# Kernel tuning notes

Hardware: AMD Instinct MI355X
Metric: run time of the kernel (lower is better)

Reference implementation:

```python
import jax, jax.numpy as jnp
import numpy as np

VOCAB = 50257
D_MODEL = 1024
TOKENS = 4096
K = 64


def setup_inputs() -> dict:
    key = jax.random.key(0)
    k1, k2, k3 = jax.random.split(key, 3)
    x = jax.random.normal(k1, (TOKENS, D_MODEL), dtype=jnp.float32)
    b = jax.random.normal(k2, (VOCAB, D_MODEL), dtype=jnp.float32)
    target = jax.random.randint(k3, (TOKENS,), 0, VOCAB, dtype=jnp.int64)
    return {"x": x, "b": b, "target": target, "k": K}


def reference(x, b, target, k):
    # faiss.knn_gpu with default METRIC_L2 returns the k SMALLEST squared-L2
    # distances D between each query row of x [tokens, d] and the database
    # rows of b [vocab, d]. target is unused in the original forward.
    x_sq = jnp.sum(x * x, axis=1, keepdims=True)          # [tokens, 1]
    b_sq = jnp.sum(b * b, axis=1)                          # [vocab]
    dist = x_sq + b_sq[None, :] - 2.0 * (x @ b.T)          # [tokens, vocab]
    # top-k smallest distances == top-k largest of -dist (sorted ascending)
    neg_d, _ = jax.lax.top_k(-dist, k)                     # [tokens, k]
    return -neg_d
```

## Files before the change

### kernel.cpp

```cpp
#include <hip/hip_runtime.h>
#include <hip/hip_bf16.h>
#include <stdint.h>

#define TOKENS 4096
#define DMODEL 1024
#define VOCAB  50257
#define KSEL   64
#define BM 128
#define BN 128
#define BK 64
#define MTILES (TOKENS / BM)
#define NSPLIT_A 16
#define COLS_A   128
#define SAMPLE_END (NSPLIT_A * COLS_A)
#define NSPLIT_B 16
#define COLS_B (VOCAB - SAMPLE_END)
#define COLS_PER ((COLS_B + NSPLIT_B - 1) / NSPLIT_B)
#define SEG 256
#define CAP 56
#define MERGE_THR 17
#define TSZ (BM * BK)
#define INF __builtin_inff()

typedef unsigned short u16;
typedef long i64;
typedef __attribute__((ext_vector_type(4))) float f32x4;

#define GLOAD16(gp, lp) __builtin_amdgcn_global_load_lds( \
    (const __attribute__((address_space(1))) void*)(gp),  \
    (__attribute__((address_space(3))) void*)(lp), 16, 0, 0)
#define GLOAD4(gp, lp) __builtin_amdgcn_global_load_lds(  \
    (const __attribute__((address_space(1))) void*)(gp),  \
    (__attribute__((address_space(3))) void*)(lp), 4, 0, 0)

#define WAITB(N) do { asm volatile("s_waitcnt vmcnt(" #N ")" ::: "memory"); \
                      __builtin_amdgcn_s_barrier(); } while (0)
#define LBAR() do { asm volatile("s_waitcnt lgkmcnt(0)" ::: "memory"); \
                    __builtin_amdgcn_s_barrier(); } while (0)
#define DRAIN_VM() asm volatile("s_waitcnt vmcnt(0)" ::: "memory")

__global__ __launch_bounds__(256) void prep_kernel(
    const float* __restrict__ x, const float* __restrict__ b,
    uint8_t* __restrict__ xh, uint8_t* __restrict__ bh,
    float* __restrict__ xsq, float* __restrict__ bsq) {
  int row = blockIdx.x;
  int tid = threadIdx.x;
  const float* src;
  uint8_t* dst;
  float* nrm;
  int r;
  if (row < TOKENS) {
    r = row; src = x + (size_t)r * DMODEL; dst = xh + (size_t)r * DMODEL; nrm = xsq;
  } else {
    r = row - TOKENS; src = b + (size_t)r * DMODEL; dst = bh + (size_t)r * DMODEL; nrm = bsq;
  }
  float4 v = reinterpret_cast<const float4*>(src)[tid];
  float s = v.x * v.x + v.y * v.y + v.z * v.z + v.w * v.w;
  uint32_t w = __builtin_amdgcn_cvt_pk_fp8_f32(v.x, v.y, 0, false);
  w = __builtin_amdgcn_cvt_pk_fp8_f32(v.z, v.w, w, true);
  reinterpret_cast<uint32_t*>(dst)[tid] = w;
#pragma unroll
  for (int j = 1; j < 64; j <<= 1) s += __shfl_xor(s, j);
  __shared__ float acc4[4];
  if ((tid & 63) == 0) acc4[tid >> 6] = s;
  __syncthreads();
  if (tid == 0) nrm[r] = acc4[0] + acc4[1] + acc4[2] + acc4[3];
}

__device__ __attribute__((noinline)) float merge_row(float lstv, const float* cb, int cnt) {
  const int lane = threadIdx.x & 63;
  float v0 = (lane < cnt) ? cb[lane] : INF;
#pragma unroll
  for (int k = 2; k <= 64; k <<= 1) {
#pragma unroll
    for (int j = k >> 1; j > 0; j >>= 1) {
      float p = __shfl_xor(v0, j);
      bool keepmin = (((lane & j) == 0) == ((lane & k) == 0));
      v0 = keepmin ? fminf(v0, p) : fmaxf(v0, p);
    }
  }
  float rev = __shfl(v0, 63 - lane);
  float m = fminf(lstv, rev);
#pragma unroll
  for (int j = 32; j > 0; j >>= 1) {
    float p = __shfl_xor(m, j);
    m = ((lane & j) == 0) ? fminf(m, p) : fmaxf(m, p);
  }
  return m;
}

__device__ __forceinline__ float merge64(float a, float b, int lane) {
  float rev = __shfl(b, 63 - lane);
  float m = fminf(a, rev);
#pragma unroll
  for (int j = 32; j > 0; j >>= 1) {
    float p = __shfl_xor(m, j);
    m = ((lane & j) == 0) ? fminf(m, p) : fmaxf(m, p);
  }
  return m;
}

#define STAGE_STEP(BB, KS) do {                        \
    GLOAD16(a_src + (KS), &As[(BB) + wave * 1024]);    \
    GLOAD16(b_src + (KS), &Bs[(BB) + wave * 1024]);    \
  } while (0)

#define MFMA8(a0_, a1_, b0_, b1_, b2_, b3_)                                           \
    acc[0][0] = __builtin_amdgcn_mfma_f32_16x16x32_fp8_fp8(a0_, b0_, acc[0][0], 0, 0, 0); \
    acc[0][1] = __builtin_amdgcn_mfma_f32_16x16x32_fp8_fp8(a0_, b1_, acc[0][1], 0, 0, 0); \
    acc[0][2] = __builtin_amdgcn_mfma_f32_16x16x32_fp8_fp8(a0_, b2_, acc[0][2], 0, 0, 0); \
    acc[0][3] = __builtin_amdgcn_mfma_f32_16x16x32_fp8_fp8(a0_, b3_, acc[0][3], 0, 0, 0); \
    acc[1][0] = __builtin_amdgcn_mfma_f32_16x16x32_fp8_fp8(a1_, b0_, acc[1][0], 0, 0, 0); \
    acc[1][1] = __builtin_amdgcn_mfma_f32_16x16x32_fp8_fp8(a1_, b1_, acc[1][1], 0, 0, 0); \
    acc[1][2] = __builtin_amdgcn_mfma_f32_16x16x32_fp8_fp8(a1_, b2_, acc[1][2], 0, 0, 0); \
    acc[1][3] = __builtin_amdgcn_mfma_f32_16x16x32_fp8_fp8(a1_, b3_, acc[1][3], 0, 0, 0);

#define LD8(arr, BB, off) (*reinterpret_cast<const i64*>(&(arr)[(BB) + (off)]))
#define COMPUTE_STEP(BB) do {                                                  \
    i64 a0 = LD8(As, BB, A00), a1 = LD8(As, BB, A10);                          \
    i64 b0 = LD8(Bs, BB, B00), b1 = LD8(Bs, BB, B10);                          \
    i64 b2 = LD8(Bs, BB, B20), b3 = LD8(Bs, BB, B30);                          \
    __builtin_amdgcn_s_setprio(1);                                             \
    MFMA8(a0, a1, b0, b1, b2, b3)                                              \
    __builtin_amdgcn_s_setprio(0);                                             \
    i64 a0b = LD8(As, BB, A01), a1b = LD8(As, BB, A11);                        \
    i64 b0b = LD8(Bs, BB, B01), b1b = LD8(Bs, BB, B11);                        \
    i64 b2b = LD8(Bs, BB, B21), b3b = LD8(Bs, BB, B31);                        \
    __builtin_amdgcn_s_setprio(1);                                             \
    MFMA8(a0b, a1b, b0b, b1b, b2b, b3b)                                        \
    __builtin_amdgcn_s_setprio(0);                                             \
  } while (0)

#define GEOM_COMMON                                                            \
  const int g4 = lane >> 4, fr = lane & 15;                                    \
  const int wm = wave >> 1, wn = wave & 1;                                     \
  const int rj = g4 * 4;                                                       \
  auto po = [&](int row, int c) {                                              \
    return row * 64 + ((((c >> 4) ^ ((row >> 1) & 3)) << 4) | (c & 15));       \
  };                                                                           \
  const int c0 = g4 * 8, c1 = 32 + g4 * 8;                                     \
  const int rA0 = wm * 32 + fr, rA1 = rA0 + 16;                                \
  const int rB0 = wn * 64 + fr, rB1 = rB0 + 16, rB2 = rB0 + 32, rB3 = rB0 + 48;\
  const int A00 = po(rA0, c0), A01 = po(rA0, c1);                              \
  const int A10 = po(rA1, c0), A11 = po(rA1, c1);                              \
  const int B00 = po(rB0, c0), B01 = po(rB0, c1);                              \
  const int B10 = po(rB1, c0), B11 = po(rB1, c1);                              \
  const int B20 = po(rB2, c0), B21 = po(rB2, c1);                              \
  const int B30 = po(rB3, c0), B31 = po(rB3, c1);

#define K_PIPELINE3()                                                           \
    _Pragma("unroll 1")                                                         \
    for (int i = 0; i < 4; ++i) {                                               \
      const int ksb = i * 192;                                                  \
      WAITB(2); STAGE_STEP(2 * TSZ, ksb + 128); COMPUTE_STEP(0);                \
      WAITB(2); STAGE_STEP(0,       ksb + 192); COMPUTE_STEP(TSZ);              \
      WAITB(2); STAGE_STEP(TSZ,     ksb + 256); COMPUTE_STEP(2 * TSZ);          \
    }                                                                           \
    WAITB(2); STAGE_STEP(2 * TSZ, 896); COMPUTE_STEP(0);                        \
    WAITB(2); STAGE_STEP(0,       960); COMPUTE_STEP(TSZ);                      \
    WAITB(2);                           COMPUTE_STEP(2 * TSZ);                  \
    WAITB(0);                           COMPUTE_STEP(0);

#define K_PIPELINE4()                                                           \
    _Pragma("unroll 1")                                                         \
    for (int i = 0; i < 3; ++i) {                                               \
      const int ksb = i * 256;                                                  \
      WAITB(4); STAGE_STEP(3 * TSZ, ksb + 192); COMPUTE_STEP(0);                \
      WAITB(4); STAGE_STEP(0,       ksb + 256); COMPUTE_STEP(TSZ);              \
      WAITB(4); STAGE_STEP(TSZ,     ksb + 320); COMPUTE_STEP(2 * TSZ);          \
      WAITB(4); STAGE_STEP(2 * TSZ, ksb + 384); COMPUTE_STEP(3 * TSZ);          \
    }                                                                           \
    WAITB(4); STAGE_STEP(3 * TSZ, 960); COMPUTE_STEP(0);              \
    WAITB(4);                           COMPUTE_STEP(TSZ);            \
    WAITB(2);                           COMPUTE_STEP(2 * TSZ);        \
    WAITB(0);                           COMPUTE_STEP(3 * TSZ);

__global__ __launch_bounds__(512, 4) void gemm_topk_sample(
    const uint8_t* __restrict__ xh, const uint8_t* __restrict__ bh,
    const float* __restrict__ xsq, const float* __restrict__ bsqg,
    float* __restrict__ parts) {
  __shared__ uint8_t As[3 * TSZ];
  __shared__ uint8_t Bs[3 * TSZ];
  __shared__ float cbuf[BM][CAP];
  __shared__ float tau[BM];
  __shared__ int   ccnt[BM];
  __shared__ float xsq_s[BM];

  const int tid  = threadIdx.x;
  const int lane = tid & 63;
  const int wave = tid >> 6;
  const int xcd = blockIdx.x & 7, idx = blockIdx.x >> 3;
  const int mt  = xcd * 4 + (idx & 3);
  const int ns  = idx >> 2;

  const int mrow0 = mt * BM;
  const int col0  = ns * COLS_A;
  const int col1  = col0 + COLS_A;

  const int stg_row = wave * 16 + (lane >> 2);
  const int stg_gran = ((lane & 3) ^ ((lane >> 3) & 3)) << 4;
  const uint8_t* a_src = xh + (size_t)(mrow0 + stg_row) * DMODEL + stg_gran;
  const uint8_t* b_src = bh + (size_t)(col0 + stg_row) * DMODEL + stg_gran;

  if (tid < BM) {
    xsq_s[tid] = xsq[mrow0 + tid];
    tau[tid] = INF;
    ccnt[tid] = 0;
  }
  STAGE_STEP(0, 0);
  STAGE_STEP(TSZ, BK);

  float lst[16];
#pragma unroll
  for (int i = 0; i < 16; ++i) lst[i] = INF;

  GEOM_COMMON
  const int r0 = wm * 32 + wn * 16;

  const int cbase = col0;
  f32x4 acc[2][4];
#pragma unroll
  for (int i = 0; i < 2; ++i)
#pragma unroll
    for (int j = 0; j < 4; ++j) acc[i][j] = (f32x4){0.f, 0.f, 0.f, 0.f};

  K_PIPELINE3()

#pragma unroll
  for (int p = 0; p < 4; ++p) {
    if (wn == (p & 1)) {
#pragma unroll
      for (int f2 = 0; f2 < 2; ++f2) {
        const int fn = (p >> 1) * 2 + f2;
        const int c = cbase + wn * 64 + fn * 16 + fr;
        const float bq = bsqg[c];
#pragma unroll
        for (int fm = 0; fm < 2; ++fm) {
#pragma unroll
          for (int j = 0; j < 4; ++j) {
            const int rl = wm * 32 + fm * 16 + rj + j;
            const float dist = xsq_s[rl] + bq - 2.0f * acc[fm][fn][j];
            if (dist < tau[rl]) {
              int ix = atomicAdd(&ccnt[rl], 1);
              if (ix < CAP) cbuf[rl][ix] = dist;
            }
          }
        }
      }
    }
    LBAR();
    const bool force = (p == 3);
#pragma unroll
    for (int rl16 = 0; rl16 < 16; ++rl16) {
      const int r = r0 + rl16;
      const int cnt = ccnt[r];
      if (cnt >= MERGE_THR || (force && cnt > 0)) {
        float m = merge_row(lst[rl16], &cbuf[r][0], cnt);
        lst[rl16] = m;
        if (lane == 63) { tau[r] = m; ccnt[r] = 0; }
      }
    }
    LBAR();
  }

#pragma unroll
  for (int rl16 = 0; rl16 < 16; ++rl16) {
    parts[(size_t)(mrow0 + r0 + rl16) * (NSPLIT_A * KSEL) + ns * KSEL + lane] = lst[rl16];
  }
}

__global__ __launch_bounds__(256) void tau_reduce_kernel(
    const float* __restrict__ parts, float* __restrict__ sample64) {
  const int lane = threadIdx.x & 63;
  const int row = blockIdx.x * 4 + (threadIdx.x >> 6);
  float v[16];
#pragma unroll
  for (int i = 0; i < 16; ++i)
    v[i] = parts[(size_t)row * (NSPLIT_A * KSEL) + i * KSEL + lane];
#pragma unroll
  for (int i = 0; i < 8; ++i) v[i] = merge64(v[i], v[i + 8], lane);
#pragma unroll
  for (int i = 0; i < 4; ++i) v[i] = merge64(v[i], v[i + 4], lane);
#pragma unroll
  for (int i = 0; i < 2; ++i) v[i] = merge64(v[i], v[i + 2], lane);
  v[0] = merge64(v[0], v[1], lane);
  sample64[(size_t)row * KSEL + lane] = v[0];
}

__global__ __launch_bounds__(512, 4) void gemm_filter_kernel(
    const uint8_t* __restrict__ xh, const uint8_t* __restrict__ bh,
    const float* __restrict__ xsq, const float* __restrict__ bsqg,
    const float* __restrict__ sample64,
    float* __restrict__ gcand, int* __restrict__ gcnt) {
  __shared__ uint8_t As[4 * TSZ];
  __shared__ uint8_t Bs[4 * TSZ];
  __shared__ float bsq_s[2][BN];
  __shared__ float xsq_s[BM];
  __shared__ float tau_s[BM];
  __shared__ int   svcnt[BM];

  const int tid  = threadIdx.x;
  const int lane = tid & 63;
  const int wave = tid >> 6;
  const int xcd = blockIdx.x & 7, idx = blockIdx.x >> 3;
  const int mt  = xcd * 4 + (idx & 3);
  const int ns  = idx >> 2;

  const int mrow0 = mt * BM;
  const int col0  = SAMPLE_END + ns * COLS_PER;
  const int col1  = (col0 + COLS_PER < VOCAB) ? (col0 + COLS_PER) : VOCAB;
  const int nchunk = (col1 - col0 + BN - 1) / BN;

  const int stg_row = wave * 16 + (lane >> 2);
  const int stg_gran = ((lane & 3) ^ ((lane >> 3) & 3)) << 4;
  const uint8_t* a_src = xh + (size_t)(mrow0 + stg_row) * DMODEL + stg_gran;
  int gc0 = col0 + stg_row; if (gc0 > VOCAB - 1) gc0 = VOCAB - 1;
  const uint8_t* b_src = bh + (size_t)gc0 * DMODEL + stg_gran;

#define STAGE_BSQ(CC) do {                                              \
    int c_ = col0 + (CC) * BN + lane;                                   \
    int cA_ = (c_ < VOCAB) ? c_ : (VOCAB - 1);                          \
    int cB_ = (c_ + 64 < VOCAB) ? (c_ + 64) : (VOCAB - 1);              \
    GLOAD4(bsqg + cA_, &bsq_s[(CC) & 1][0]);                            \
    GLOAD4(bsqg + cB_, &bsq_s[(CC) & 1][64]);                           \
  } while (0)

  if (tid < BM) {
    xsq_s[tid] = xsq[mrow0 + tid];
    tau_s[tid] = sample64[(size_t)(mrow0 + tid) * KSEL + (KSEL - 1)];
    svcnt[tid] = 0;
  }
  STAGE_BSQ(0);
  STAGE_STEP(0, 0);
  STAGE_STEP(TSZ, BK);
  STAGE_STEP(2 * TSZ, 2 * BK);

  GEOM_COMMON
  float* seg_base = gcand + (size_t)mrow0 * (NSPLIT_B * SEG) + (size_t)ns * SEG;

#pragma unroll 1
  for (int ch = 0; ch < nchunk; ++ch) {
    const int cbase = col0 + ch * BN;
    f32x4 acc[2][4];
#pragma unroll
    for (int i = 0; i < 2; ++i)
#pragma unroll
      for (int j = 0; j < 4; ++j) acc[i][j] = (f32x4){0.f, 0.f, 0.f, 0.f};

    K_PIPELINE4()

#pragma unroll
    for (int fn = 0; fn < 4; ++fn) {
      const int c = cbase + wn * 64 + fn * 16 + fr;
      const bool cv = (c < col1);
      const float bq = bsq_s[ch & 1][wn * 64 + fn * 16 + fr];
#pragma unroll
      for (int fm = 0; fm < 2; ++fm) {
#pragma unroll
        for (int j = 0; j < 4; ++j) {
          const int rl = wm * 32 + fm * 16 + rj + j;
          const float dist = xsq_s[rl] + bq - 2.0f * acc[fm][fn][j];
          if (cv && dist < tau_s[rl]) {
            int ix = atomicAdd(&svcnt[rl], 1);
            if (ix < SEG)
              seg_base[(size_t)rl * (NSPLIT_B * SEG) + ix] = dist;
          }
        }
      }
    }
    DRAIN_VM();
    if (ch + 1 < nchunk) {
      STAGE_BSQ(ch + 1);
      int gcn = cbase + BN + stg_row;
      if (gcn > VOCAB - 1) gcn = VOCAB - 1;
      b_src = bh + (size_t)gcn * DMODEL + stg_gran;
      STAGE_STEP(0, 0);
      STAGE_STEP(TSZ, BK);
      STAGE_STEP(2 * TSZ, 2 * BK);
    }
  }

  LBAR();
  if (tid < BM) {
    int c = svcnt[tid]; if (c > SEG) c = SEG;
    gcnt[(size_t)(mrow0 + tid) * NSPLIT_B + ns] = c;
  }
}

__global__ __launch_bounds__(256) void select_kernel(
    const float* __restrict__ gcand, const int* __restrict__ gcnt,
    const float* __restrict__ sample64, float* __restrict__ out) {
  const int lane = threadIdx.x & 63;
  const int row = blockIdx.x * 4 + (threadIdx.x >> 6);
  float lst = sample64[(size_t)row * KSEL + lane];
#pragma unroll 1
  for (int s = 0; s < NSPLIT_B; ++s) {
    int cnt = gcnt[(size_t)row * NSPLIT_B + s];
    const float* src = gcand + (size_t)row * (NSPLIT_B * SEG) + (size_t)s * SEG;
#pragma unroll 1
    for (int base = 0; base < cnt; base += 64) {
      int n = cnt - base; if (n > 64) n = 64;
      lst = merge_row(lst, src + base, n);
    }
  }
  out[(size_t)row * KSEL + lane] = lst;
}

extern "C" void kernel_launch(void* const* d_in, const int* in_sizes, int n_in,
                              void* d_out, int out_size, void* d_ws, size_t ws_size,
                              hipStream_t stream) {
  const float* x = (const float*)d_in[0];
  const float* b = (const float*)d_in[1];
  float* out = (float*)d_out;
  char* ws = (char*)d_ws;

  size_t off = 0;
  uint8_t* xh = (uint8_t*)(ws + off); off += (size_t)TOKENS * DMODEL;
  uint8_t* bh = (uint8_t*)(ws + off); off += (size_t)VOCAB * DMODEL;
  off = (off + 255) & ~(size_t)255;
  float* xsq = (float*)(ws + off); off += (size_t)TOKENS * sizeof(float);
  float* bsq = (float*)(ws + off); off += (((size_t)VOCAB * sizeof(float)) + 255) & ~(size_t)255;
  float* sample64 = (float*)(ws + off); off += (size_t)TOKENS * KSEL * sizeof(float);
  int* gcnt = (int*)(ws + off); off += (size_t)TOKENS * NSPLIT_B * sizeof(int);
  float* parts = (float*)(ws + off); off += (size_t)TOKENS * NSPLIT_A * KSEL * sizeof(float);
  float* gcand = (float*)(ws + off); off += (size_t)TOKENS * NSPLIT_B * SEG * sizeof(float);

  prep_kernel<<<TOKENS + VOCAB, 256, 0, stream>>>(x, b, xh, bh, xsq, bsq);
  gemm_topk_sample<<<MTILES * NSPLIT_A, 512, 0, stream>>>(xh, bh, xsq, bsq, parts);
  tau_reduce_kernel<<<TOKENS / 4, 256, 0, stream>>>(parts, sample64);
  gemm_filter_kernel<<<MTILES * NSPLIT_B, 512, 0, stream>>>(xh, bh, xsq, bsq, sample64, gcand, gcnt);
  select_kernel<<<TOKENS / 4, 256, 0, stream>>>(gcand, gcnt, sample64, out);
}
```

Before: 612.6 us.

## Enlarge filter GEMM M-tile to 256 rows with 3-stage pipeline and 32 column splits

The filter GEMM kernel now uses 256-row A tiles with each wave computing a 64x64 sub-tile (4x4 MFMA fragments), so each B tile is reused across twice as many query rows. The K pipeline drops from 4 to 3 LDS stages to fit the larger A buffer, and the vocab split doubles to 32 with per-segment candidate capacity halved to 128. This cuts B-matrix reloads and raises MFMA work per LDS read, at the cost of more accumulator registers per wave at the same launch bounds. The smaller segment capacity also raises the risk of candidate overflow. An extra barrier is added before restaging each chunk.

```diff
diff --git a/kernel.cpp b/kernel.cpp
--- a/kernel.cpp
+++ b/kernel.cpp
@@ -6,20 +6,22 @@
 #define DMODEL 1024
 #define VOCAB  50257
 #define KSEL   64
-#define BM 128
 #define BN 128
 #define BK 64
-#define MTILES (TOKENS / BM)
+#define BMS 128
 #define NSPLIT_A 16
 #define COLS_A   128
 #define SAMPLE_END (NSPLIT_A * COLS_A)
-#define NSPLIT_B 16
+#define TSZ (BMS * BK)
+#define BMF 256
+#define NSPLIT_B 32
 #define COLS_B (VOCAB - SAMPLE_END)
 #define COLS_PER ((COLS_B + NSPLIT_B - 1) / NSPLIT_B)
-#define SEG 256
+#define ATSZ (BMF * BK)
+#define BTSZ (BN * BK)
+#define SEG 128
 #define CAP 56
 #define MERGE_THR 17
-#define TSZ (BM * BK)
 #define INF __builtin_inff()
 
 typedef unsigned short u16;
@@ -131,13 +133,15 @@
     __builtin_amdgcn_s_setprio(0);                                             \
   } while (0)
 
+#define PO_DEF auto po = [&](int row, int c) {                                 \
+    return row * 64 + ((((c >> 4) ^ ((row >> 1) & 3)) << 4) | (c & 15));       \
+  };
+
 #define GEOM_COMMON                                                            \
   const int g4 = lane >> 4, fr = lane & 15;                                    \
   const int wm = wave >> 1, wn = wave & 1;                                     \
   const int rj = g4 * 4;                                                       \
-  auto po = [&](int row, int c) {                                              \
-    return row * 64 + ((((c >> 4) ^ ((row >> 1) & 3)) << 4) | (c & 15));       \
-  };                                                                           \
+  PO_DEF                                                                       \
   const int c0 = g4 * 8, c1 = 32 + g4 * 8;                                     \
   const int rA0 = wm * 32 + fr, rA1 = rA0 + 16;                                \
   const int rB0 = wn * 64 + fr, rB1 = rB0 + 16, rB2 = rB0 + 32, rB3 = rB0 + 48;\
@@ -161,30 +165,16 @@
     WAITB(2);                           COMPUTE_STEP(2 * TSZ);                  \
     WAITB(0);                           COMPUTE_STEP(0);
 
-#define K_PIPELINE4()                                                           \
-    _Pragma("unroll 1")                                                         \
-    for (int i = 0; i < 3; ++i) {                                               \
-      const int ksb = i * 256;                                                  \
-      WAITB(4); STAGE_STEP(3 * TSZ, ksb + 192); COMPUTE_STEP(0);                \
-      WAITB(4); STAGE_STEP(0,       ksb + 256); COMPUTE_STEP(TSZ);              \
-      WAITB(4); STAGE_STEP(TSZ,     ksb + 320); COMPUTE_STEP(2 * TSZ);          \
-      WAITB(4); STAGE_STEP(2 * TSZ, ksb + 384); COMPUTE_STEP(3 * TSZ);          \
-    }                                                                           \
-    WAITB(4); STAGE_STEP(3 * TSZ, 960); COMPUTE_STEP(0);              \
-    WAITB(4);                           COMPUTE_STEP(TSZ);            \
-    WAITB(2);                           COMPUTE_STEP(2 * TSZ);        \
-    WAITB(0);                           COMPUTE_STEP(3 * TSZ);
-
 __global__ __launch_bounds__(512, 4) void gemm_topk_sample(
     const uint8_t* __restrict__ xh, const uint8_t* __restrict__ bh,
     const float* __restrict__ xsq, const float* __restrict__ bsqg,
     float* __restrict__ parts) {
   __shared__ uint8_t As[3 * TSZ];
   __shared__ uint8_t Bs[3 * TSZ];
-  __shared__ float cbuf[BM][CAP];
-  __shared__ float tau[BM];
-  __shared__ int   ccnt[BM];
-  __shared__ float xsq_s[BM];
+  __shared__ float cbuf[BMS][CAP];
+  __shared__ float tau[BMS];
+  __shared__ int   ccnt[BMS];
+  __shared__ float xsq_s[BMS];
 
   const int tid  = threadIdx.x;
   const int lane = tid & 63;
@@ -193,16 +183,15 @@
   const int mt  = xcd * 4 + (idx & 3);
   const int ns  = idx >> 2;
 
-  const int mrow0 = mt * BM;
+  const int mrow0 = mt * BMS;
   const int col0  = ns * COLS_A;
-  const int col1  = col0 + COLS_A;
 
   const int stg_row = wave * 16 + (lane >> 2);
   const int stg_gran = ((lane & 3) ^ ((lane >> 3) & 3)) << 4;
   const uint8_t* a_src = xh + (size_t)(mrow0 + stg_row) * DMODEL + stg_gran;
   const uint8_t* b_src = bh + (size_t)(col0 + stg_row) * DMODEL + stg_gran;
 
-  if (tid < BM) {
+  if (tid < BMS) {
     xsq_s[tid] = xsq[mrow0 + tid];
     tau[tid] = INF;
     ccnt[tid] = 0;
@@ -287,34 +276,82 @@
   sample64[(size_t)row * KSEL + lane] = v[0];
 }
 
+#define STAGE_F(N, KS) do {                                      \
+    GLOAD16(a_src0 + (KS), &As[(N) * ATSZ + wave * 2048]);       \
+    GLOAD16(a_src1 + (KS), &As[(N) * ATSZ + wave * 2048 + 1024]);\
+    GLOAD16(b_src  + (KS), &Bs[(N) * BTSZ + wave * 1024]);       \
+  } while (0)
+
+#define MFMA16(AS, BS)                                                              \
+    _Pragma("unroll")                                                               \
+    for (int ms = 0; ms < 4; ++ms) {                                                \
+      acc[ms][0] = __builtin_amdgcn_mfma_f32_16x16x32_fp8_fp8(AS[ms], BS[0], acc[ms][0], 0, 0, 0); \
+      acc[ms][1] = __builtin_amdgcn_mfma_f32_16x16x32_fp8_fp8(AS[ms], BS[1], acc[ms][1], 0, 0, 0); \
+      acc[ms][2] = __builtin_amdgcn_mfma_f32_16x16x32_fp8_fp8(AS[ms], BS[2], acc[ms][2], 0, 0, 0); \
+      acc[ms][3] = __builtin_amdgcn_mfma_f32_16x16x32_fp8_fp8(AS[ms], BS[3], acc[ms][3], 0, 0, 0); \
+    }
+
+#define COMPUTE_F(N) do {                                                      \
+    const int ba = (N) * ATSZ, bb = (N) * BTSZ;                                \
+    i64 af[4], bf[4];                                                          \
+    af[0] = LD8(As, ba, AF00); af[1] = LD8(As, ba, AF10);                      \
+    af[2] = LD8(As, ba, AF20); af[3] = LD8(As, ba, AF30);                      \
+    bf[0] = LD8(Bs, bb, BF00); bf[1] = LD8(Bs, bb, BF10);                      \
+    bf[2] = LD8(Bs, bb, BF20); bf[3] = LD8(Bs, bb, BF30);                      \
+    __builtin_amdgcn_s_setprio(1);                                             \
+    MFMA16(af, bf)                                                             \
+    __builtin_amdgcn_s_setprio(0);                                             \
+    af[0] = LD8(As, ba, AF01); af[1] = LD8(As, ba, AF11);                      \
+    af[2] = LD8(As, ba, AF21); af[3] = LD8(As, ba, AF31);                      \
+    bf[0] = LD8(Bs, bb, BF01); bf[1] = LD8(Bs, bb, BF11);                      \
+    bf[2] = LD8(Bs, bb, BF21); bf[3] = LD8(Bs, bb, BF31);                      \
+    __builtin_amdgcn_s_setprio(1);                                             \
+    MFMA16(af, bf)                                                             \
+    __builtin_amdgcn_s_setprio(0);                                             \
+  } while (0)
+
+#define K_PIPELINE_F()                                                          \
+    _Pragma("unroll 1")                                                         \
+    for (int i = 0; i < 4; ++i) {                                               \
+      const int ksb = i * 192;                                                  \
+      WAITB(3); STAGE_F(2, ksb + 128); COMPUTE_F(0);                            \
+      WAITB(3); STAGE_F(0, ksb + 192); COMPUTE_F(1);                            \
+      WAITB(3); STAGE_F(1, ksb + 256); COMPUTE_F(2);                            \
+    }                                                                           \
+    WAITB(3); STAGE_F(2, 896); COMPUTE_F(0);                \
+    WAITB(3); STAGE_F(0, 960); COMPUTE_F(1);                \
+    WAITB(3);                  COMPUTE_F(2);                           \
+    WAITB(0);                  COMPUTE_F(0);
+
 __global__ __launch_bounds__(512, 4) void gemm_filter_kernel(
     const uint8_t* __restrict__ xh, const uint8_t* __restrict__ bh,
     const float* __restrict__ xsq, const float* __restrict__ bsqg,
     const float* __restrict__ sample64,
     float* __restrict__ gcand, int* __restrict__ gcnt) {
-  __shared__ uint8_t As[4 * TSZ];
-  __shared__ uint8_t Bs[4 * TSZ];
+  __shared__ uint8_t As[3 * ATSZ];
+  __shared__ uint8_t Bs[3 * BTSZ];
   __shared__ float bsq_s[2][BN];
-  __shared__ float xsq_s[BM];
-  __shared__ float tau_s[BM];
-  __shared__ int   svcnt[BM];
+  __shared__ float xsq_s[BMF];
+  __shared__ float tau_s[BMF];
+  __shared__ int   svcnt[BMF];
 
   const int tid  = threadIdx.x;
   const int lane = tid & 63;
   const int wave = tid >> 6;
   const int xcd = blockIdx.x & 7, idx = blockIdx.x >> 3;
-  const int mt  = xcd * 4 + (idx & 3);
-  const int ns  = idx >> 2;
-
-  const int mrow0 = mt * BM;
+  const int mt  = xcd * 2 + (idx & 1);
+  const int ns  = idx >> 1;
+
+  const int mrow0 = mt * BMF;
   const int col0  = SAMPLE_END + ns * COLS_PER;
   const int col1  = (col0 + COLS_PER < VOCAB) ? (col0 + COLS_PER) : VOCAB;
   const int nchunk = (col1 - col0 + BN - 1) / BN;
 
-  const int stg_row = wave * 16 + (lane >> 2);
+  const int stg_r16 = lane >> 2;
   const int stg_gran = ((lane & 3) ^ ((lane >> 3) & 3)) << 4;
-  const uint8_t* a_src = xh + (size_t)(mrow0 + stg_row) * DMODEL + stg_gran;
-  int gc0 = col0 + stg_row; if (gc0 > VOCAB - 1) gc0 = VOCAB - 1;
+  const uint8_t* a_src0 = xh + (size_t)(mrow0 + wave * 32 + stg_r16) * DMODEL + stg_gran;
+  const uint8_t* a_src1 = a_src0 + (size_t)16 * DMODEL;
+  int gc0 = col0 + wave * 16 + stg_r16; if (gc0 > VOCAB - 1) gc0 = VOCAB - 1;
   const uint8_t* b_src = bh + (size_t)gc0 * DMODEL + stg_gran;
 
 #define STAGE_BSQ(CC) do {                                              \
@@ -325,41 +362,53 @@
     GLOAD4(bsqg + cB_, &bsq_s[(CC) & 1][64]);                           \
   } while (0)
 
-  if (tid < BM) {
+  if (tid < BMF) {
     xsq_s[tid] = xsq[mrow0 + tid];
     tau_s[tid] = sample64[(size_t)(mrow0 + tid) * KSEL + (KSEL - 1)];
     svcnt[tid] = 0;
   }
   STAGE_BSQ(0);
-  STAGE_STEP(0, 0);
-  STAGE_STEP(TSZ, BK);
-  STAGE_STEP(2 * TSZ, 2 * BK);
-
-  GEOM_COMMON
+  STAGE_F(0, 0);
+  STAGE_F(1, BK);
+
+  const int g4 = lane >> 4, fr = lane & 15;
+  const int wm = wave >> 1, wn = wave & 1;
+  const int rj = g4 * 4;
+  PO_DEF
+  const int c0 = g4 * 8, c1 = 32 + g4 * 8;
+  const int AF00 = po(wm * 64 +  0 + fr, c0), AF01 = po(wm * 64 +  0 + fr, c1);
+  const int AF10 = po(wm * 64 + 16 + fr, c0), AF11 = po(wm * 64 + 16 + fr, c1);
+  const int AF20 = po(wm * 64 + 32 + fr, c0), AF21 = po(wm * 64 + 32 + fr, c1);
+  const int AF30 = po(wm * 64 + 48 + fr, c0), AF31 = po(wm * 64 + 48 + fr, c1);
+  const int BF00 = po(wn * 64 +  0 + fr, c0), BF01 = po(wn * 64 +  0 + fr, c1);
+  const int BF10 = po(wn * 64 + 16 + fr, c0), BF11 = po(wn * 64 + 16 + fr, c1);
+  const int BF20 = po(wn * 64 + 32 + fr, c0), BF21 = po(wn * 64 + 32 + fr, c1);
+  const int BF30 = po(wn * 64 + 48 + fr, c0), BF31 = po(wn * 64 + 48 + fr, c1);
+
   float* seg_base = gcand + (size_t)mrow0 * (NSPLIT_B * SEG) + (size_t)ns * SEG;
 
 #pragma unroll 1
   for (int ch = 0; ch < nchunk; ++ch) {
     const int cbase = col0 + ch * BN;
-    f32x4 acc[2][4];
-#pragma unroll
-    for (int i = 0; i < 2; ++i)
+    f32x4 acc[4][4];
+#pragma unroll
+    for (int i = 0; i < 4; ++i)
 #pragma unroll
       for (int j = 0; j < 4; ++j) acc[i][j] = (f32x4){0.f, 0.f, 0.f, 0.f};
 
-    K_PIPELINE4()
-
-#pragma unroll
-    for (int fn = 0; fn < 4; ++fn) {
-      const int c = cbase + wn * 64 + fn * 16 + fr;
+    K_PIPELINE_F()
+
+#pragma unroll
+    for (int nf = 0; nf < 4; ++nf) {
+      const int c = cbase + wn * 64 + nf * 16 + fr;
       const bool cv = (c < col1);
-      const float bq = bsq_s[ch & 1][wn * 64 + fn * 16 + fr];
-#pragma unroll
-      for (int fm = 0; fm < 2; ++fm) {
+      const float bq = bsq_s[ch & 1][wn * 64 + nf * 16 + fr];
+#pragma unroll
+      for (int ms = 0; ms < 4; ++ms) {
 #pragma unroll
         for (int j = 0; j < 4; ++j) {
-          const int rl = wm * 32 + fm * 16 + rj + j;
-          const float dist = xsq_s[rl] + bq - 2.0f * acc[fm][fn][j];
+          const int rl = wm * 64 + ms * 16 + rj + j;
+          const float dist = xsq_s[rl] + bq - 2.0f * acc[ms][nf][j];
           if (cv && dist < tau_s[rl]) {
             int ix = atomicAdd(&svcnt[rl], 1);
             if (ix < SEG)
@@ -369,19 +418,19 @@
       }
     }
     DRAIN_VM();
+    LBAR();
     if (ch + 1 < nchunk) {
       STAGE_BSQ(ch + 1);
-      int gcn = cbase + BN + stg_row;
+      int gcn = col0 + (ch + 1) * BN + wave * 16 + stg_r16;
       if (gcn > VOCAB - 1) gcn = VOCAB - 1;
       b_src = bh + (size_t)gcn * DMODEL + stg_gran;
-      STAGE_STEP(0, 0);
-      STAGE_STEP(TSZ, BK);
-      STAGE_STEP(2 * TSZ, 2 * BK);
+      STAGE_F(0, 0);
+      STAGE_F(1, BK);
     }
   }
 
   LBAR();
-  if (tid < BM) {
+  if (tid < BMF) {
     int c = svcnt[tid]; if (c > SEG) c = SEG;
     gcnt[(size_t)(mrow0 + tid) * NSPLIT_B + ns] = c;
   }
@@ -426,8 +475,8 @@
   float* gcand = (float*)(ws + off); off += (size_t)TOKENS * NSPLIT_B * SEG * sizeof(float);
 
   prep_kernel<<<TOKENS + VOCAB, 256, 0, stream>>>(x, b, xh, bh, xsq, bsq);
-  gemm_topk_sample<<<MTILES * NSPLIT_A, 512, 0, stream>>>(xh, bh, xsq, bsq, parts);
+  gemm_topk_sample<<<(TOKENS / BMS) * NSPLIT_A, 512, 0, stream>>>(xh, bh, xsq, bsq, parts);
   tau_reduce_kernel<<<TOKENS / 4, 256, 0, stream>>>(parts, sample64);
-  gemm_filter_kernel<<<MTILES * NSPLIT_B, 512, 0, stream>>>(xh, bh, xsq, bsq, sample64, gcand, gcnt);
+  gemm_filter_kernel<<<(TOKENS / BMF) * NSPLIT_B, 512, 0, stream>>>(xh, bh, xsq, bsq, sample64, gcand, gcnt);
   select_kernel<<<TOKENS / 4, 256, 0, stream>>>(gcand, gcnt, sample64, out);
 }
```

After: 818.7 us. 1.34x slower.

## Widen filter grid to 24 column splits with 3-stage pipeline and new tile mapping

Applied to the files above, without the earlier changes.

The filter GEMM's vocabulary split grows from 16 to 24, so its grid becomes 768 blocks instead of 512. Its K pipeline drops from four LDS stages to three, which frees shared memory and may allow more resident blocks. The block-to-tile mapping across XCDs is rearranged to suit the new grid, and each segment's candidate capacity is halved to 128. Halving the capacity adds risk, because rows with many candidates in one segment may now overflow and drop entries, and an extra barrier is inserted before restaging.

```diff
diff --git a/kernel.cpp b/kernel.cpp
--- a/kernel.cpp
+++ b/kernel.cpp
@@ -6,17 +6,16 @@
 #define DMODEL 1024
 #define VOCAB  50257
 #define KSEL   64
-#define BM 128
 #define BN 128
 #define BK 64
-#define MTILES (TOKENS / BM)
+#define BM 128
 #define NSPLIT_A 16
 #define COLS_A   128
 #define SAMPLE_END (NSPLIT_A * COLS_A)
-#define NSPLIT_B 16
+#define NSPLIT_B 24
 #define COLS_B (VOCAB - SAMPLE_END)
 #define COLS_PER ((COLS_B + NSPLIT_B - 1) / NSPLIT_B)
-#define SEG 256
+#define SEG 128
 #define CAP 56
 #define MERGE_THR 17
 #define TSZ (BM * BK)
@@ -131,13 +130,15 @@
     __builtin_amdgcn_s_setprio(0);                                             \
   } while (0)
 
+#define PO_DEF auto po = [&](int row, int c) {                                 \
+    return row * 64 + ((((c >> 4) ^ ((row >> 1) & 3)) << 4) | (c & 15));       \
+  };
+
 #define GEOM_COMMON                                                            \
   const int g4 = lane >> 4, fr = lane & 15;                                    \
   const int wm = wave >> 1, wn = wave & 1;                                     \
   const int rj = g4 * 4;                                                       \
-  auto po = [&](int row, int c) {                                              \
-    return row * 64 + ((((c >> 4) ^ ((row >> 1) & 3)) << 4) | (c & 15));       \
-  };                                                                           \
+  PO_DEF                                                                       \
   const int c0 = g4 * 8, c1 = 32 + g4 * 8;                                     \
   const int rA0 = wm * 32 + fr, rA1 = rA0 + 16;                                \
   const int rB0 = wn * 64 + fr, rB1 = rB0 + 16, rB2 = rB0 + 32, rB3 = rB0 + 48;\
@@ -161,20 +162,6 @@
     WAITB(2);                           COMPUTE_STEP(2 * TSZ);                  \
     WAITB(0);                           COMPUTE_STEP(0);
 
-#define K_PIPELINE4()                                                           \
-    _Pragma("unroll 1")                                                         \
-    for (int i = 0; i < 3; ++i) {                                               \
-      const int ksb = i * 256;                                                  \
-      WAITB(4); STAGE_STEP(3 * TSZ, ksb + 192); COMPUTE_STEP(0);                \
-      WAITB(4); STAGE_STEP(0,       ksb + 256); COMPUTE_STEP(TSZ);              \
-      WAITB(4); STAGE_STEP(TSZ,     ksb + 320); COMPUTE_STEP(2 * TSZ);          \
-      WAITB(4); STAGE_STEP(2 * TSZ, ksb + 384); COMPUTE_STEP(3 * TSZ);          \
-    }                                                                           \
-    WAITB(4); STAGE_STEP(3 * TSZ, 960); COMPUTE_STEP(0);              \
-    WAITB(4);                           COMPUTE_STEP(TSZ);            \
-    WAITB(2);                           COMPUTE_STEP(2 * TSZ);        \
-    WAITB(0);                           COMPUTE_STEP(3 * TSZ);
-
 __global__ __launch_bounds__(512, 4) void gemm_topk_sample(
     const uint8_t* __restrict__ xh, const uint8_t* __restrict__ bh,
     const float* __restrict__ xsq, const float* __restrict__ bsqg,
@@ -195,7 +182,6 @@
 
   const int mrow0 = mt * BM;
   const int col0  = ns * COLS_A;
-  const int col1  = col0 + COLS_A;
 
   const int stg_row = wave * 16 + (lane >> 2);
   const int stg_gran = ((lane & 3) ^ ((lane >> 3) & 3)) << 4;
@@ -292,8 +278,8 @@
     const float* __restrict__ xsq, const float* __restrict__ bsqg,
     const float* __restrict__ sample64,
     float* __restrict__ gcand, int* __restrict__ gcnt) {
-  __shared__ uint8_t As[4 * TSZ];
-  __shared__ uint8_t Bs[4 * TSZ];
+  __shared__ uint8_t As[3 * TSZ];
+  __shared__ uint8_t Bs[3 * TSZ];
   __shared__ float bsq_s[2][BN];
   __shared__ float xsq_s[BM];
   __shared__ float tau_s[BM];
@@ -303,8 +289,8 @@
   const int lane = tid & 63;
   const int wave = tid >> 6;
   const int xcd = blockIdx.x & 7, idx = blockIdx.x >> 3;
-  const int mt  = xcd * 4 + (idx & 3);
-  const int ns  = idx >> 2;
+  const int mt  = ((xcd >> 1) << 3) + (idx & 7);
+  const int ns  = (xcd & 1) * 12 + (idx >> 3);
 
   const int mrow0 = mt * BM;
   const int col0  = SAMPLE_END + ns * COLS_PER;
@@ -333,7 +319,6 @@
   STAGE_BSQ(0);
   STAGE_STEP(0, 0);
   STAGE_STEP(TSZ, BK);
-  STAGE_STEP(2 * TSZ, 2 * BK);
 
   GEOM_COMMON
   float* seg_base = gcand + (size_t)mrow0 * (NSPLIT_B * SEG) + (size_t)ns * SEG;
@@ -347,7 +332,7 @@
 #pragma unroll
       for (int j = 0; j < 4; ++j) acc[i][j] = (f32x4){0.f, 0.f, 0.f, 0.f};
 
-    K_PIPELINE4()
+    K_PIPELINE3()
 
 #pragma unroll
     for (int fn = 0; fn < 4; ++fn) {
@@ -369,14 +354,14 @@
       }
     }
     DRAIN_VM();
+    LBAR();
     if (ch + 1 < nchunk) {
       STAGE_BSQ(ch + 1);
-      int gcn = cbase + BN + stg_row;
+      int gcn = col0 + (ch + 1) * BN + stg_row;
       if (gcn > VOCAB - 1) gcn = VOCAB - 1;
       b_src = bh + (size_t)gcn * DMODEL + stg_gran;
       STAGE_STEP(0, 0);
       STAGE_STEP(TSZ, BK);
-      STAGE_STEP(2 * TSZ, 2 * BK);
     }
   }
 
@@ -426,8 +411,8 @@
   float* gcand = (float*)(ws + off); off += (size_t)TOKENS * NSPLIT_B * SEG * sizeof(float);
 
   prep_kernel<<<TOKENS + VOCAB, 256, 0, stream>>>(x, b, xh, bh, xsq, bsq);
-  gemm_topk_sample<<<MTILES * NSPLIT_A, 512, 0, stream>>>(xh, bh, xsq, bsq, parts);
+  gemm_topk_sample<<<(TOKENS / BM) * NSPLIT_A, 512, 0, stream>>>(xh, bh, xsq, bsq, parts);
   tau_reduce_kernel<<<TOKENS / 4, 256, 0, stream>>>(parts, sample64);
-  gemm_filter_kernel<<<MTILES * NSPLIT_B, 512, 0, stream>>>(xh, bh, xsq, bsq, sample64, gcand, gcnt);
+  gemm_filter_kernel<<<(TOKENS / BM) * NSPLIT_B, 512, 0, stream>>>(xh, bh, xsq, bsq, sample64, gcand, gcnt);
   select_kernel<<<TOKENS / 4, 256, 0, stream>>>(gcand, gcnt, sample64, out);
 }
```

Measured after the change: 657.3 us. 1.07x slower.

## Write raw sample distances to global and select top-k in separate reduce kernel

Applied to the files above, without the earlier changes.

The sample GEMM kernel no longer keeps a per-tile top-64 in shared memory with atomics, thresholds and bitonic merges. It now writes every distance in the 2048-column sample to a global buffer. A rewritten reduce kernel then merges each row's 2048 distances in 64-wide chunks using the bitonic merge_row routine. This takes the serial, barrier-heavy selection out of the GEMM epilogue, at the cost of about 32 MB of extra global writes and reads and a longer serial merge loop per row.

```diff
diff --git a/kernel.cpp b/kernel.cpp
--- a/kernel.cpp
+++ b/kernel.cpp
@@ -6,10 +6,9 @@
 #define DMODEL 1024
 #define VOCAB  50257
 #define KSEL   64
-#define BM 128
 #define BN 128
 #define BK 64
-#define MTILES (TOKENS / BM)
+#define BM 128
 #define NSPLIT_A 16
 #define COLS_A   128
 #define SAMPLE_END (NSPLIT_A * COLS_A)
@@ -17,8 +16,6 @@
 #define COLS_B (VOCAB - SAMPLE_END)
 #define COLS_PER ((COLS_B + NSPLIT_B - 1) / NSPLIT_B)
 #define SEG 256
-#define CAP 56
-#define MERGE_THR 17
 #define TSZ (BM * BK)
 #define INF __builtin_inff()
 
@@ -81,17 +78,6 @@
   }
   float rev = __shfl(v0, 63 - lane);
   float m = fminf(lstv, rev);
-#pragma unroll
-  for (int j = 32; j > 0; j >>= 1) {
-    float p = __shfl_xor(m, j);
-    m = ((lane & j) == 0) ? fminf(m, p) : fmaxf(m, p);
-  }
-  return m;
-}
-
-__device__ __forceinline__ float merge64(float a, float b, int lane) {
-  float rev = __shfl(b, 63 - lane);
-  float m = fminf(a, rev);
 #pragma unroll
   for (int j = 32; j > 0; j >>= 1) {
     float p = __shfl_xor(m, j);
@@ -131,13 +117,15 @@
     __builtin_amdgcn_s_setprio(0);                                             \
   } while (0)
 
+#define PO_DEF auto po = [&](int row, int c) {                                 \
+    return row * 64 + ((((c >> 4) ^ ((row >> 1) & 3)) << 4) | (c & 15));       \
+  };
+
 #define GEOM_COMMON                                                            \
   const int g4 = lane >> 4, fr = lane & 15;                                    \
   const int wm = wave >> 1, wn = wave & 1;                                     \
   const int rj = g4 * 4;                                                       \
-  auto po = [&](int row, int c) {                                              \
-    return row * 64 + ((((c >> 4) ^ ((row >> 1) & 3)) << 4) | (c & 15));       \
-  };                                                                           \
+  PO_DEF                                                                       \
   const int c0 = g4 * 8, c1 = 32 + g4 * 8;                                     \
   const int rA0 = wm * 32 + fr, rA1 = rA0 + 16;                                \
   const int rB0 = wn * 64 + fr, rB1 = rB0 + 16, rB2 = rB0 + 32, rB3 = rB0 + 48;\
@@ -175,15 +163,12 @@
     WAITB(2);                           COMPUTE_STEP(2 * TSZ);        \
     WAITB(0);                           COMPUTE_STEP(3 * TSZ);
 
-__global__ __launch_bounds__(512, 4) void gemm_topk_sample(
+__global__ __launch_bounds__(512, 4) void gemm_sample_dist(
     const uint8_t* __restrict__ xh, const uint8_t* __restrict__ bh,
     const float* __restrict__ xsq, const float* __restrict__ bsqg,
-    float* __restrict__ parts) {
+    float* __restrict__ sdist) {
   __shared__ uint8_t As[3 * TSZ];
   __shared__ uint8_t Bs[3 * TSZ];
-  __shared__ float cbuf[BM][CAP];
-  __shared__ float tau[BM];
-  __shared__ int   ccnt[BM];
   __shared__ float xsq_s[BM];
 
   const int tid  = threadIdx.x;
@@ -195,29 +180,18 @@
 
   const int mrow0 = mt * BM;
   const int col0  = ns * COLS_A;
-  const int col1  = col0 + COLS_A;
 
   const int stg_row = wave * 16 + (lane >> 2);
   const int stg_gran = ((lane & 3) ^ ((lane >> 3) & 3)) << 4;
   const uint8_t* a_src = xh + (size_t)(mrow0 + stg_row) * DMODEL + stg_gran;
   const uint8_t* b_src = bh + (size_t)(col0 + stg_row) * DMODEL + stg_gran;
 
-  if (tid < BM) {
-    xsq_s[tid] = xsq[mrow0 + tid];
-    tau[tid] = INF;
-    ccnt[tid] = 0;
-  }
+  if (tid < BM) xsq_s[tid] = xsq[mrow0 + tid];
   STAGE_STEP(0, 0);
   STAGE_STEP(TSZ, BK);
 
-  float lst[16];
-#pragma unroll
-  for (int i = 0; i < 16; ++i) lst[i] = INF;
-
   GEOM_COMMON
-  const int r0 = wm * 32 + wn * 16;
-
-  const int cbase = col0;
+
   f32x4 acc[2][4];
 #pragma unroll
   for (int i = 0; i < 2; ++i)
@@ -227,64 +201,31 @@
   K_PIPELINE3()
 
 #pragma unroll
-  for (int p = 0; p < 4; ++p) {
-    if (wn == (p & 1)) {
-#pragma unroll
-      for (int f2 = 0; f2 < 2; ++f2) {
-        const int fn = (p >> 1) * 2 + f2;
-        const int c = cbase + wn * 64 + fn * 16 + fr;
-        const float bq = bsqg[c];
-#pragma unroll
-        for (int fm = 0; fm < 2; ++fm) {
-#pragma unroll
-          for (int j = 0; j < 4; ++j) {
-            const int rl = wm * 32 + fm * 16 + rj + j;
-            const float dist = xsq_s[rl] + bq - 2.0f * acc[fm][fn][j];
-            if (dist < tau[rl]) {
-              int ix = atomicAdd(&ccnt[rl], 1);
-              if (ix < CAP) cbuf[rl][ix] = dist;
-            }
-          }
-        }
+  for (int fn = 0; fn < 4; ++fn) {
+    const int c = col0 + wn * 64 + fn * 16 + fr;
+    const float bq = bsqg[c];
+#pragma unroll
+    for (int fm = 0; fm < 2; ++fm) {
+#pragma unroll
+      for (int j = 0; j < 4; ++j) {
+        const int rl = wm * 32 + fm * 16 + rj + j;
+        sdist[(size_t)(mrow0 + rl) * SAMPLE_END + c] =
+            xsq_s[rl] + bq - 2.0f * acc[fm][fn][j];
       }
     }
-    LBAR();
-    const bool force = (p == 3);
-#pragma unroll
-    for (int rl16 = 0; rl16 < 16; ++rl16) {
-      const int r = r0 + rl16;
-      const int cnt = ccnt[r];
-      if (cnt >= MERGE_THR || (force && cnt > 0)) {
-        float m = merge_row(lst[rl16], &cbuf[r][0], cnt);
-        lst[rl16] = m;
-        if (lane == 63) { tau[r] = m; ccnt[r] = 0; }
-      }
-    }
-    LBAR();
-  }
-
-#pragma unroll
-  for (int rl16 = 0; rl16 < 16; ++rl16) {
-    parts[(size_t)(mrow0 + r0 + rl16) * (NSPLIT_A * KSEL) + ns * KSEL + lane] = lst[rl16];
-  }
-}
-
-__global__ __launch_bounds__(256) void tau_reduce_kernel(
-    const float* __restrict__ parts, float* __restrict__ sample64) {
+  }
+}
+
+__global__ __launch_bounds__(256) void sample_reduce_kernel(
+    const float* __restrict__ sdist, float* __restrict__ sample64) {
   const int lane = threadIdx.x & 63;
   const int row = blockIdx.x * 4 + (threadIdx.x >> 6);
-  float v[16];
-#pragma unroll
-  for (int i = 0; i < 16; ++i)
-    v[i] = parts[(size_t)row * (NSPLIT_A * KSEL) + i * KSEL + lane];
-#pragma unroll
-  for (int i = 0; i < 8; ++i) v[i] = merge64(v[i], v[i + 8], lane);
-#pragma unroll
-  for (int i = 0; i < 4; ++i) v[i] = merge64(v[i], v[i + 4], lane);
-#pragma unroll
-  for (int i = 0; i < 2; ++i) v[i] = merge64(v[i], v[i + 2], lane);
-  v[0] = merge64(v[0], v[1], lane);
-  sample64[(size_t)row * KSEL + lane] = v[0];
+  const float* src = sdist + (size_t)row * SAMPLE_END;
+  float lst = INF;
+#pragma unroll 1
+  for (int base = 0; base < SAMPLE_END; base += 64)
+    lst = merge_row(lst, src + base, 64);
+  sample64[(size_t)row * KSEL + lane] = lst;
 }
 
 __global__ __launch_bounds__(512, 4) void gemm_filter_kernel(
@@ -422,12 +363,12 @@
   float* bsq = (float*)(ws + off); off += (((size_t)VOCAB * sizeof(float)) + 255) & ~(size_t)255;
   float* sample64 = (float*)(ws + off); off += (size_t)TOKENS * KSEL * sizeof(float);
   int* gcnt = (int*)(ws + off); off += (size_t)TOKENS * NSPLIT_B * sizeof(int);
-  float* parts = (float*)(ws + off); off += (size_t)TOKENS * NSPLIT_A * KSEL * sizeof(float);
+  float* sdist = (float*)(ws + off); off += (size_t)TOKENS * SAMPLE_END * sizeof(float);
   float* gcand = (float*)(ws + off); off += (size_t)TOKENS * NSPLIT_B * SEG * sizeof(float);
 
   prep_kernel<<<TOKENS + VOCAB, 256, 0, stream>>>(x, b, xh, bh, xsq, bsq);
-  gemm_topk_sample<<<MTILES * NSPLIT_A, 512, 0, stream>>>(xh, bh, xsq, bsq, parts);
-  tau_reduce_kernel<<<TOKENS / 4, 256, 0, stream>>>(parts, sample64);
-  gemm_filter_kernel<<<MTILES * NSPLIT_B, 512, 0, stream>>>(xh, bh, xsq, bsq, sample64, gcand, gcnt);
+  gemm_sample_dist<<<(TOKENS / BM) * NSPLIT_A, 512, 0, stream>>>(xh, bh, xsq, bsq, sdist);
+  sample_reduce_kernel<<<TOKENS / 4, 256, 0, stream>>>(sdist, sample64);
+  gemm_filter_kernel<<<(TOKENS / BM) * NSPLIT_B, 512, 0, stream>>>(xh, bh, xsq, bsq, sample64, gcand, gcnt);
   select_kernel<<<TOKENS / 4, 256, 0, stream>>>(gcand, gcnt, sample64, out);
 }
```

After: 544.2 us. 1.13x faster.
